# Kernel tuning notes

Measured on AMD Instinct MI355X. Metric: run time of the kernel, lower is better.

Reference implementation:

```python
import jax, jax.numpy as jnp
import numpy as np

ALPHA = 0.1
B = 500_000
EMBED = 64
HIDDEN = 128
IN_DIM = 27 + 3 + EMBED  # 94

def _gelu(x):
    return jax.nn.gelu(x, approximate=False)  # torch.nn.GELU default = exact erf

def setup_inputs() -> dict:
    key = jax.random.key(0)
    ks = jax.random.split(key, 8)
    s = 0.05
    return {
        "F": jnp.eye(3, dtype=jnp.float32)[None] + 0.1 * jax.random.normal(ks[0], (B, 3, 3), jnp.float32),
        "latent_weight": jax.random.normal(ks[1], (1024, EMBED), jnp.float32),
        "W1": s * jax.random.normal(ks[2], (IN_DIM, HIDDEN), jnp.float32), "b1": jnp.zeros((HIDDEN,), jnp.float32),
        "W2": s * jax.random.normal(ks[3], (HIDDEN, HIDDEN), jnp.float32), "b2": jnp.zeros((HIDDEN,), jnp.float32),
        "W3": s * jax.random.normal(ks[4], (HIDDEN, HIDDEN), jnp.float32), "b3": jnp.zeros((HIDDEN,), jnp.float32),
        "W4": s * jax.random.normal(ks[5], (HIDDEN, HIDDEN), jnp.float32), "b4": jnp.zeros((HIDDEN,), jnp.float32),
        "W5": s * jax.random.normal(ks[6], (HIDDEN, 9), jnp.float32), "b5": jnp.zeros((9,), jnp.float32),
        "traj_ids": jnp.asarray(7, dtype=jnp.int32),
    }

def reference(F, latent_weight, W1, b1, W2, b2, W3, b3, W4, b4, W5, b5, traj_ids):
    n = F.shape[0]
    # Batched 3x3 SVD: F = U diag(s) Vh  (torch.svd returns V; Vh = V^T here)
    U, sigma, Vh = jnp.linalg.svd(F, full_matrices=False)
    R = jnp.matmul(U, Vh)  # [n,3,3] rotation
    lat = jnp.broadcast_to(latent_weight[traj_ids][None, :], (n, latent_weight.shape[1]))
    inv = jnp.concatenate(
        [F.reshape(n, 9), U.reshape(n, 9), sigma, Vh.reshape(n, 9), lat], axis=1)  # [n, 30+embed]
    h = _gelu(inv @ W1 + b1)
    h = _gelu(h @ W2 + b2)
    h = _gelu(h @ W3 + b3)
    h = _gelu(h @ W4 + b4)
    x = (h @ W5 + b5).reshape(n, 3, 3)
    x = 0.5 * (x + jnp.swapaxes(x, 1, 2))  # symmetrize
    return ALPHA * jnp.matmul(R, x) + F
```

## Files before the change

kernel.cpp:

```cpp
#include <hip/hip_runtime.h>


typedef short bf16x8 __attribute__((ext_vector_type(8)));
typedef float f32x4 __attribute__((ext_vector_type(4)));
typedef float f32x2 __attribute__((ext_vector_type(2)));
typedef unsigned int u32x2 __attribute__((ext_vector_type(2)));
typedef unsigned short u16;

#define WS_L1     0
#define WS_L234   8192
#define WS_L5     106496
#define WS_B1EFF  110592
#define WS_B234   111104
#define WS_B5     112640
#define WS_NEEDED 131072

__device__ __forceinline__ float bf2f(u16 b){
  union { unsigned int u; float f; } v; v.u = ((unsigned int)b) << 16; return v.f;
}
__device__ __forceinline__ u16 f2bf(float f){
  union { float f; unsigned int u; } v; v.f = f;
  unsigned int x = v.u;
  return (u16)((x + 0x7fffu + ((x >> 16) & 1u)) >> 16);
}
__device__ __forceinline__ unsigned int pack2bf(float f0, float f1){
  union { float f; unsigned int u; } a, b; a.f = f0; b.f = f1;
  unsigned int u0 = a.u + 0x8000u;
  unsigned int u1 = b.u + 0x8000u;
#if __has_builtin(__builtin_amdgcn_perm)
  return __builtin_amdgcn_perm(u1, u0, 0x07060302u);
#else
  return (u0 >> 16) | (u1 & 0xffff0000u);
#endif
}
template<bool B16>
__device__ __forceinline__ float ldf(const void* p, int i){
  return B16 ? bf2f(((const u16*)p)[i]) : ((const float*)p)[i];
}
template<bool B16>
__device__ __forceinline__ short ldw(const void* p, int i){
  return B16 ? (short)((const u16*)p)[i] : (short)f2bf(((const float*)p)[i]);
}
template<bool B16>
__device__ __forceinline__ void stf(void* p, int i, float v){
  if (B16) ((u16*)p)[i] = f2bf(v); else ((float*)p)[i] = v;
}

__device__ __forceinline__ float med3f(float x, float lo, float hi){
#if __has_builtin(__builtin_amdgcn_fmed3f)
  return __builtin_amdgcn_fmed3f(x, lo, hi);
#else
  return fminf(fmaxf(x, lo), hi);
#endif
}

__device__ __forceinline__ unsigned int gelu2_pack(float x0, float x1){
  const f32x2 A7 = {-2.20713e-4f, -2.20713e-4f};
  const f32x2 A5 = { 5.86695e-3f,  5.86695e-3f};
  const f32x2 A3 = {-5.99485e-2f, -5.99485e-2f};
  const f32x2 A1 = { 3.969014e-1f, 3.969014e-1f};
  const f32x2 HF = { 0.5f, 0.5f};
  f32x2 xc; xc[0] = med3f(x0, -3.4f, 3.4f); xc[1] = med3f(x1, -3.4f, 3.4f);
  f32x2 s  = xc * xc;
  f32x2 g  = s * A7 + A5;
  g = s * g + A3;
  g = s * g + A1;
  f32x2 ph = xc * g + HF;
  f32x2 xin; xin[0] = x0; xin[1] = x1;
  f32x2 y = xin * ph;
  return pack2bf(y[0], y[1]);
}

__device__ __forceinline__ int sniff_bf16(const void* Fg){
  const u16* fu = (const u16*)Fg;
  int votes = 0;
  #pragma unroll
  for (int k = 0; k < 32; ++k){
    u16 h = fu[k*18];
    votes += (h >= 0x3E00 && h < 0x4000) ? 1 : 0;
  }
  return votes >= 16;
}

template<int P, int Q, int R3>
__device__ __forceinline__ void jrot(float bm[3][3], float v[3][3]){
  float bpq = bm[P][Q];
  if (fabsf(bpq) < 1e-30f) return;
  float th = (bm[Q][Q] - bm[P][P]) / (2.0f * bpq);
  float t = copysignf(1.0f, th) / (fabsf(th) + sqrtf(1.0f + th*th));
  float c = 1.0f / sqrtf(1.0f + t*t);
  float s = t * c;
  float bpp = bm[P][P] - t*bpq;
  float bqq = bm[Q][Q] + t*bpq;
  bm[P][P] = bpp; bm[Q][Q] = bqq; bm[P][Q] = 0.0f; bm[Q][P] = 0.0f;
  float bpr = bm[P][R3], bqr = bm[Q][R3];
  float npr = c*bpr - s*bqr;
  float nqr = s*bpr + c*bqr;
  bm[P][R3] = npr; bm[R3][P] = npr;
  bm[Q][R3] = nqr; bm[R3][Q] = nqr;
  #pragma unroll
  for (int i = 0; i < 3; ++i){
    float vp = v[i][P], vq = v[i][Q];
    v[i][P] = c*vp - s*vq;
    v[i][Q] = s*vp + c*vq;
  }
}

__device__ __forceinline__ void svd3(const float Fm[9],
                                     float u[3][3], float sg[3], float vt[3][3]){
  float bm[3][3];
  #pragma unroll
  for (int i = 0; i < 3; ++i)
    #pragma unroll
    for (int j = i; j < 3; ++j){
      float acc = Fm[0*3+i]*Fm[0*3+j] + Fm[1*3+i]*Fm[1*3+j] + Fm[2*3+i]*Fm[2*3+j];
      bm[i][j] = acc; bm[j][i] = acc;
    }
  float v[3][3] = {{1.f,0.f,0.f},{0.f,1.f,0.f},{0.f,0.f,1.f}};
  #pragma unroll
  for (int sweep = 0; sweep < 5; ++sweep){
    jrot<0,1,2>(bm, v);
    jrot<0,2,1>(bm, v);
    jrot<1,2,0>(bm, v);
  }
  float lam0 = bm[0][0], lam1 = bm[1][1], lam2 = bm[2][2];
  #define CSWAP(la, lb, A, Bc) if ((la) < (lb)) { float t_ = la; la = lb; lb = t_; \
    for (int i_ = 0; i_ < 3; ++i_){ float w_ = v[i_][A]; v[i_][A] = v[i_][Bc]; v[i_][Bc] = w_; } }
  CSWAP(lam0, lam1, 0, 1);
  CSWAP(lam0, lam2, 0, 2);
  CSWAP(lam1, lam2, 1, 2);
  #undef CSWAP
  float a[3][3];
  #pragma unroll
  for (int c = 0; c < 3; ++c)
    #pragma unroll
    for (int r = 0; r < 3; ++r)
      a[r][c] = Fm[r*3+0]*v[0][c] + Fm[r*3+1]*v[1][c] + Fm[r*3+2]*v[2][c];
  float s1 = sqrtf(a[0][0]*a[0][0] + a[1][0]*a[1][0] + a[2][0]*a[2][0]);
  float inv1 = 1.0f / fmaxf(s1, 1e-30f);
  u[0][0] = a[0][0]*inv1; u[1][0] = a[1][0]*inv1; u[2][0] = a[2][0]*inv1;
  float d12 = u[0][0]*a[0][1] + u[1][0]*a[1][1] + u[2][0]*a[2][1];
  float w20 = a[0][1] - d12*u[0][0], w21 = a[1][1] - d12*u[1][0], w22 = a[2][1] - d12*u[2][0];
  float s2 = sqrtf(w20*w20 + w21*w21 + w22*w22);
  float inv2 = 1.0f / fmaxf(s2, 1e-30f);
  u[0][1] = w20*inv2; u[1][1] = w21*inv2; u[2][1] = w22*inv2;
  float d13 = u[0][0]*a[0][2] + u[1][0]*a[1][2] + u[2][0]*a[2][2];
  float d23 = u[0][1]*a[0][2] + u[1][1]*a[1][2] + u[2][1]*a[2][2];
  float w30 = a[0][2] - d13*u[0][0] - d23*u[0][1];
  float w31 = a[1][2] - d13*u[1][0] - d23*u[1][1];
  float w32 = a[2][2] - d13*u[2][0] - d23*u[2][1];
  float s3 = sqrtf(w30*w30 + w31*w31 + w32*w32);
  if (s3 > 1e-12f){
    float inv3 = 1.0f / s3;
    u[0][2] = w30*inv3; u[1][2] = w31*inv3; u[2][2] = w32*inv3;
  } else {
    float c0 = u[1][0]*u[2][1] - u[2][0]*u[1][1];
    float c1 = u[2][0]*u[0][1] - u[0][0]*u[2][1];
    float c2 = u[0][0]*u[1][1] - u[1][0]*u[0][1];
    float dt = c0*a[0][2] + c1*a[1][2] + c2*a[2][2];
    float sgn = (dt < 0.0f) ? -1.0f : 1.0f;
    u[0][2] = c0*sgn; u[1][2] = c1*sgn; u[2][2] = c2*sgn;
    s3 = fabsf(dt);
  }
  sg[0] = s1; sg[1] = s2; sg[2] = s3;
  #pragma unroll
  for (int i = 0; i < 3; ++i)
    #pragma unroll
    for (int j = 0; j < 3; ++j)
      vt[i][j] = v[j][i];
}

template<bool B16>
__device__ void prep_body(
  const void* latg, const void* w1g, const void* b1g,
  const void* w2g, const void* b2g, const void* w3g, const void* b3g,
  const void* w4g, const void* b4g, const void* w5g, const void* b5g,
  const int* trajg, char* ws)
{
  const int tid = threadIdx.x, lane = tid & 63, wv = tid >> 6;
  const int quad = lane >> 4, l15 = lane & 15;
  const int blk = blockIdx.x;
  if (blk < 27){
    const int wr = blk*4 + wv;
    bf16x8 frag;
    if (wr < 8){
      const int ntg = wr;
      #pragma unroll
      for (int j = 0; j < 8; ++j)
        frag[j] = ldw<B16>(w1g, (quad*8 + j)*128 + ntg*16 + l15);
      *(bf16x8*)(ws + WS_L1 + (size_t)(wr*64 + lane)*16) = frag;
    } else if (wr < 104){
      const int idx = wr - 8, layer = idx >> 5, rem = idx & 31;
      const int ntg = rem >> 2, ks = rem & 3;
      const void* wg = (layer == 0) ? w2g : ((layer == 1) ? w3g : w4g);
      #pragma unroll
      for (int j = 0; j < 8; ++j)
        frag[j] = ldw<B16>(wg, (ks*32 + quad*8 + j)*128 + ntg*16 + l15);
      *(bf16x8*)(ws + WS_L234 + (size_t)(idx*64 + lane)*16) = frag;
    } else {
      const int ks = wr - 104;
      #pragma unroll
      for (int j = 0; j < 8; ++j)
        frag[j] = (l15 < 9) ? ldw<B16>(w5g, (ks*32 + quad*8 + j)*9 + l15) : (short)0;
      *(bf16x8*)(ws + WS_L5 + (size_t)(ks*64 + lane)*16) = frag;
    }
  } else {
    if (tid < 128){
      const int t7 = trajg[0];
      float acc = ldf<B16>(b1g, tid);
      for (int j = 0; j < 64; ++j)
        acc += ldf<B16>(latg, t7*64 + j) * ldf<B16>(w1g, (30 + j)*128 + tid);
      ((float*)(ws + WS_B1EFF))[tid] = acc;
    } else {
      const int n = tid - 128;
      ((float*)(ws + WS_B234))[0*128 + n] = ldf<B16>(b2g, n);
      ((float*)(ws + WS_B234))[1*128 + n] = ldf<B16>(b3g, n);
      ((float*)(ws + WS_B234))[2*128 + n] = ldf<B16>(b4g, n);
      if (n < 16) ((float*)(ws + WS_B5))[n] = (n < 9) ? ldf<B16>(b5g, n) : 0.0f;
    }
  }
}

__global__ __launch_bounds__(256)
void fproj_prep_kernel(
  const void* Fg, const void* latg, const void* w1g, const void* b1g,
  const void* w2g, const void* b2g, const void* w3g, const void* b3g,
  const void* w4g, const void* b4g, const void* w5g, const void* b5g,
  const int* __restrict__ trajg, char* ws)
{
  if (sniff_bf16(Fg))
    prep_body<true >(latg, w1g, b1g, w2g, b2g, w3g, b3g, w4g, b4g, w5g, b5g, trajg, ws);
  else
    prep_body<false>(latg, w1g, b1g, w2g, b2g, w3g, b3g, w4g, b4g, w5g, b5g, trajg, ws);
}

template<bool B16, bool WS>
__device__ __forceinline__ void mlp_layer128(
    u16 (&Hbuf)[128][136],
    const void* __restrict__ Wg, const void* __restrict__ bg,
    const char* __restrict__ wsW, const float* __restrict__ bf32,
    int wv, int lane)
{
  const int l15  = lane & 15;
  const int quad = lane >> 4;
  const int kb   = quad * 8;
  f32x4 bb[2];
  #pragma unroll
  for (int nt = 0; nt < 2; ++nt){
    const int n0 = wv*32 + nt*16 + quad*4;
    if (WS) bb[nt] = *(const f32x4*)(bf32 + n0);
    else { bb[nt][0]=ldf<B16>(bg,n0); bb[nt][1]=ldf<B16>(bg,n0+1);
           bb[nt][2]=ldf<B16>(bg,n0+2); bb[nt][3]=ldf<B16>(bg,n0+3); }
  }
  bf16x8 Wf[2][4];
  #pragma unroll
  for (int nt = 0; nt < 2; ++nt){
    const int ntg = wv*2 + nt;
    #pragma unroll
    for (int ks = 0; ks < 4; ++ks){
      if (WS){
        Wf[nt][ks] = *(const bf16x8*)(wsW + (size_t)((ntg*4 + ks)*64 + lane)*16);
      } else {
        bf16x8 bv;
        #pragma unroll
        for (int j = 0; j < 8; ++j)
          bv[j] = ldw<B16>(Wg, (ks*32 + kb + j)*128 + ntg*16 + l15);
        Wf[nt][ks] = bv;
      }
    }
  }
  f32x4 acc[8][2];
  #pragma unroll
  for (int mt = 0; mt < 8; ++mt){
    const u16* hp = &Hbuf[mt*16 + l15][kb];
    bf16x8 a0 = *(const bf16x8*)(hp);
    bf16x8 a1 = *(const bf16x8*)(hp + 32);
    bf16x8 a2 = *(const bf16x8*)(hp + 64);
    bf16x8 a3 = *(const bf16x8*)(hp + 96);
    #pragma unroll
    for (int nt = 0; nt < 2; ++nt){
      f32x4 c = bb[nt];
      c = __builtin_amdgcn_mfma_f32_16x16x32_bf16(Wf[nt][0], a0, c, 0,0,0);
      c = __builtin_amdgcn_mfma_f32_16x16x32_bf16(Wf[nt][1], a1, c, 0,0,0);
      c = __builtin_amdgcn_mfma_f32_16x16x32_bf16(Wf[nt][2], a2, c, 0,0,0);
      c = __builtin_amdgcn_mfma_f32_16x16x32_bf16(Wf[nt][3], a3, c, 0,0,0);
      acc[mt][nt] = c;
    }
  }
  __syncthreads();
  #pragma unroll
  for (int nt = 0; nt < 2; ++nt){
    const int n0 = wv*32 + nt*16 + quad*4;
    #pragma unroll
    for (int mt = 0; mt < 8; ++mt){
      f32x4 c = acc[mt][nt];
      u32x2 pk;
      pk[0] = gelu2_pack(c[0], c[1]);
      pk[1] = gelu2_pack(c[2], c[3]);
      *(u32x2*)&Hbuf[mt*16 + l15][n0] = pk;
    }
  }
  __syncthreads();
}

template<bool B16, bool WS>
__device__ void fproj_body(
  const void* Fg, const void* latg,
  const void* w1g, const void* b1g, const void* w2g, const void* b2g,
  const void* w3g, const void* b3g, const void* w4g, const void* b4g,
  const void* w5g, const void* b5g,
  const int* trajg, void* outg, int ntot, const char* ws,
  u16 (&Hbuf)[128][136], float* b1lds)
{
  const int tid  = threadIdx.x;
  const int lane = tid & 63;
  const int wv   = tid >> 6;
  const int l15  = lane & 15;
  const int quad = lane >> 4;
  const int kb   = quad * 8;
  const int row0 = blockIdx.x * 128;

  float Freg[9];
  float Rm[3][3];

  bf16x8 Wf1[2];
  #pragma unroll
  for (int nt = 0; nt < 2; ++nt){
    const int ntg = wv*2 + nt;
    if (WS){
      Wf1[nt] = *(const bf16x8*)(ws + WS_L1 + (size_t)(ntg*64 + lane)*16);
    } else {
      bf16x8 bv;
      #pragma unroll
      for (int j = 0; j < 8; ++j)
        bv[j] = ldw<B16>(w1g, (kb + j)*128 + ntg*16 + l15);
      Wf1[nt] = bv;
    }
  }

  if (tid < 128){
    const int r = row0 + tid;
    float fv[32];
    if (r < ntot){
      float A0[9];
      #pragma unroll
      for (int k = 0; k < 9; ++k){ A0[k] = ldf<B16>(Fg, r*9 + k); Freg[k] = A0[k]; }
      float uu[3][3], ss[3], vvt[3][3];
      svd3(A0, uu, ss, vvt);
      #pragma unroll
      for (int i = 0; i < 3; ++i)
        #pragma unroll
        for (int j = 0; j < 3; ++j)
          Rm[i][j] = uu[i][0]*vvt[0][j] + uu[i][1]*vvt[1][j] + uu[i][2]*vvt[2][j];
      #pragma unroll
      for (int k = 0; k < 9; ++k) fv[k]    = A0[k];
      #pragma unroll
      for (int k = 0; k < 9; ++k) fv[9+k]  = uu[k/3][k%3];
      fv[18] = ss[0]; fv[19] = ss[1]; fv[20] = ss[2];
      #pragma unroll
      for (int k = 0; k < 9; ++k) fv[21+k] = vvt[k/3][k%3];
      fv[30] = 0.0f; fv[31] = 0.0f;
    } else {
      #pragma unroll
      for (int k = 0; k < 32; ++k) fv[k] = 0.0f;
      #pragma unroll
      for (int k = 0; k < 9; ++k) Freg[k] = 0.0f;
      #pragma unroll
      for (int i = 0; i < 3; ++i)
        #pragma unroll
        for (int j = 0; j < 3; ++j) Rm[i][j] = 0.0f;
    }
    #pragma unroll
    for (int q = 0; q < 4; ++q){
      u32x2 pk;
      pk[0] = pack2bf(fv[q*8+0], fv[q*8+1]);
      pk[1] = pack2bf(fv[q*8+2], fv[q*8+3]);
      *(u32x2*)&Hbuf[tid][q*8 + 0] = pk;
      pk[0] = pack2bf(fv[q*8+4], fv[q*8+5]);
      pk[1] = pack2bf(fv[q*8+6], fv[q*8+7]);
      *(u32x2*)&Hbuf[tid][q*8 + 4] = pk;
    }
  } else if (!WS){
    const int n = tid - 128;
    const int t7 = trajg[0];
    float acc = ldf<B16>(b1g, n);
    for (int j = 0; j < 64; ++j)
      acc += ldf<B16>(latg, t7*64 + j) * ldf<B16>(w1g, (30 + j)*128 + n);
    b1lds[n] = acc;
  }
  __syncthreads();

  {
    f32x4 bb[2];
    #pragma unroll
    for (int nt = 0; nt < 2; ++nt){
      const int n0 = wv*32 + nt*16 + quad*4;
      if (WS) bb[nt] = *(const f32x4*)((const float*)(ws + WS_B1EFF) + n0);
      else { bb[nt][0]=b1lds[n0]; bb[nt][1]=b1lds[n0+1]; bb[nt][2]=b1lds[n0+2]; bb[nt][3]=b1lds[n0+3]; }
    }
    f32x4 acc[8][2];
    #pragma unroll
    for (int mt = 0; mt < 8; ++mt){
      bf16x8 av = *(const bf16x8*)&Hbuf[mt*16 + l15][kb];
      #pragma unroll
      for (int nt = 0; nt < 2; ++nt){
        f32x4 c = bb[nt];
        c = __builtin_amdgcn_mfma_f32_16x16x32_bf16(Wf1[nt], av, c, 0,0,0);
        acc[mt][nt] = c;
      }
    }
    __syncthreads();
    #pragma unroll
    for (int nt = 0; nt < 2; ++nt){
      const int n0 = wv*32 + nt*16 + quad*4;
      #pragma unroll
      for (int mt = 0; mt < 8; ++mt){
        f32x4 c = acc[mt][nt];
        u32x2 pk;
        pk[0] = gelu2_pack(c[0], c[1]);
        pk[1] = gelu2_pack(c[2], c[3]);
        *(u32x2*)&Hbuf[mt*16 + l15][n0] = pk;
      }
    }
  }
  __syncthreads();

  const float* bf32 = (const float*)(ws + WS_B234);
  mlp_layer128<B16,WS>(Hbuf, w2g, b2g, ws + WS_L234 + 0*32768, bf32 + 0*128, wv, lane);
  mlp_layer128<B16,WS>(Hbuf, w3g, b3g, ws + WS_L234 + 1*32768, bf32 + 1*128, wv, lane);
  mlp_layer128<B16,WS>(Hbuf, w4g, b4g, ws + WS_L234 + 2*32768, bf32 + 2*128, wv, lane);

  {
    bf16x8 W5f[4];
    #pragma unroll
    for (int ks = 0; ks < 4; ++ks){
      if (WS){
        W5f[ks] = *(const bf16x8*)(ws + WS_L5 + (size_t)(ks*64 + lane)*16);
      } else {
        bf16x8 bv;
        #pragma unroll
        for (int j = 0; j < 8; ++j)
          bv[j] = (l15 < 9) ? ldw<B16>(w5g, (ks*32 + kb + j)*9 + l15) : (short)0;
        W5f[ks] = bv;
      }
    }
    f32x4 bb5;
    if (WS) bb5 = *(const f32x4*)((const float*)(ws + WS_B5) + quad*4);
    else {
      #pragma unroll
      for (int rg = 0; rg < 4; ++rg)
        bb5[rg] = (quad*4 + rg < 9) ? ldf<B16>(b5g, quad*4 + rg) : 0.0f;
    }
    #pragma unroll
    for (int t = 0; t < 2; ++t){
      const int mt = wv*2 + t;
      const u16* hp = &Hbuf[mt*16 + l15][kb];
      bf16x8 a0 = *(const bf16x8*)(hp);
      bf16x8 a1 = *(const bf16x8*)(hp + 32);
      bf16x8 a2 = *(const bf16x8*)(hp + 64);
      bf16x8 a3 = *(const bf16x8*)(hp + 96);
      f32x4 c = bb5;
      c = __builtin_amdgcn_mfma_f32_16x16x32_bf16(W5f[0], a0, c, 0,0,0);
      c = __builtin_amdgcn_mfma_f32_16x16x32_bf16(W5f[1], a1, c, 0,0,0);
      c = __builtin_amdgcn_mfma_f32_16x16x32_bf16(W5f[2], a2, c, 0,0,0);
      c = __builtin_amdgcn_mfma_f32_16x16x32_bf16(W5f[3], a3, c, 0,0,0);
      *(f32x4*)((float*)&Hbuf[mt*16 + l15][0] + quad*4) = c;
    }
  }
  __syncthreads();

  if (tid < 128){
    const int r = row0 + tid;
    if (r < ntot){
      const float* xr = (const float*)&Hbuf[tid][0];
      float x[9];
      #pragma unroll
      for (int k = 0; k < 9; ++k) x[k] = xr[k];
      float xs[3][3];
      #pragma unroll
      for (int i = 0; i < 3; ++i)
        #pragma unroll
        for (int j = 0; j < 3; ++j)
          xs[i][j] = 0.5f*(x[i*3+j] + x[j*3+i]);
      #pragma unroll
      for (int i = 0; i < 3; ++i)
        #pragma unroll
        for (int j = 0; j < 3; ++j){
          float y = Rm[i][0]*xs[0][j] + Rm[i][1]*xs[1][j] + Rm[i][2]*xs[2][j];
          stf<B16>(outg, r*9 + i*3 + j, 0.1f*y + Freg[i*3+j]);
        }
    }
  }
}

__global__ __launch_bounds__(256, 4)
void fproj_ws_kernel(
  const void* Fg, const void* latg,
  const void* w1g, const void* b1g, const void* w2g, const void* b2g,
  const void* w3g, const void* b3g, const void* w4g, const void* b4g,
  const void* w5g, const void* b5g,
  const int* __restrict__ trajg, void* outg, int ntot, const char* ws)
{
  __shared__ alignas(16) u16 Hbuf[128][136];
  if (sniff_bf16(Fg))
    fproj_body<true , true>(Fg, latg, w1g, b1g, w2g, b2g, w3g, b3g, w4g, b4g,
                            w5g, b5g, trajg, outg, ntot, ws, Hbuf, nullptr);
  else
    fproj_body<false, true>(Fg, latg, w1g, b1g, w2g, b2g, w3g, b3g, w4g, b4g,
                            w5g, b5g, trajg, outg, ntot, ws, Hbuf, nullptr);
}

__global__ __launch_bounds__(256, 4)
void fproj_plain_kernel(
  const void* Fg, const void* latg,
  const void* w1g, const void* b1g, const void* w2g, const void* b2g,
  const void* w3g, const void* b3g, const void* w4g, const void* b4g,
  const void* w5g, const void* b5g,
  const int* __restrict__ trajg, void* outg, int ntot)
{
  __shared__ alignas(16) u16 Hbuf[128][136];
  __shared__ float b1lds[128];
  if (sniff_bf16(Fg))
    fproj_body<true , false>(Fg, latg, w1g, b1g, w2g, b2g, w3g, b3g, w4g, b4g,
                             w5g, b5g, trajg, outg, ntot, nullptr, Hbuf, b1lds);
  else
    fproj_body<false, false>(Fg, latg, w1g, b1g, w2g, b2g, w3g, b3g, w4g, b4g,
                             w5g, b5g, trajg, outg, ntot, nullptr, Hbuf, b1lds);
}

extern "C" void kernel_launch(void* const* d_in, const int* in_sizes, int n_in,
                              void* d_out, int out_size, void* d_ws, size_t ws_size,
                              hipStream_t stream) {
  (void)n_in; (void)out_size;
  const int n = in_sizes[0] / 9;
  dim3 grid((n + 127) / 128), block(256);
  if (ws_size >= (size_t)WS_NEEDED){
    hipLaunchKernelGGL(fproj_prep_kernel, dim3(28), block, 0, stream,
      (const void*)d_in[0],  (const void*)d_in[1],
      (const void*)d_in[2],  (const void*)d_in[3],
      (const void*)d_in[4],  (const void*)d_in[5],
      (const void*)d_in[6],  (const void*)d_in[7],
      (const void*)d_in[8],  (const void*)d_in[9],
      (const void*)d_in[10], (const void*)d_in[11],
      (const int*)d_in[12], (char*)d_ws);
    hipLaunchKernelGGL(fproj_ws_kernel, grid, block, 0, stream,
      (const void*)d_in[0],  (const void*)d_in[1],
      (const void*)d_in[2],  (const void*)d_in[3],
      (const void*)d_in[4],  (const void*)d_in[5],
      (const void*)d_in[6],  (const void*)d_in[7],
      (const void*)d_in[8],  (const void*)d_in[9],
      (const void*)d_in[10], (const void*)d_in[11],
      (const int*)d_in[12], d_out, n, (const char*)d_ws);
  } else {
    hipLaunchKernelGGL(fproj_plain_kernel, grid, block, 0, stream,
      (const void*)d_in[0],  (const void*)d_in[1],
      (const void*)d_in[2],  (const void*)d_in[3],
      (const void*)d_in[4],  (const void*)d_in[5],
      (const void*)d_in[6],  (const void*)d_in[7],
      (const void*)d_in[8],  (const void*)d_in[9],
      (const void*)d_in[10], (const void*)d_in[11],
      (const int*)d_in[12], d_out, n);
  }
}
```

Baseline: 198.6 us.

## Replace padded LDS activation buffer with XOR-swizzled unpadded layout

The activation tile in LDS drops its 8-element row padding (136 to 128 columns). Bank conflicts are now avoided by XOR-swizzling 16-byte chunks with the row index, applied to every read and write of the buffer. The smaller LDS footprint lets the launch-bounds occupancy hint rise from 4 to 5 blocks per CU, and the GELU clamp now uses vector min/max builtins instead of fmed3. The risk is extra address arithmetic and higher register pressure under the tighter occupancy bound.

```diff
diff --git a/kernel.cpp b/kernel.cpp
--- a/kernel.cpp
+++ b/kernel.cpp
@@ -46,12 +46,8 @@
   if (B16) ((u16*)p)[i] = f2bf(v); else ((float*)p)[i] = v;
 }
 
-__device__ __forceinline__ float med3f(float x, float lo, float hi){
-#if __has_builtin(__builtin_amdgcn_fmed3f)
-  return __builtin_amdgcn_fmed3f(x, lo, hi);
-#else
-  return fminf(fmaxf(x, lo), hi);
-#endif
+__device__ __forceinline__ int swz(int r15, int boff){
+  return boff ^ (r15 << 4);
 }
 
 __device__ __forceinline__ unsigned int gelu2_pack(float x0, float x1){
@@ -60,13 +56,15 @@
   const f32x2 A3 = {-5.99485e-2f, -5.99485e-2f};
   const f32x2 A1 = { 3.969014e-1f, 3.969014e-1f};
   const f32x2 HF = { 0.5f, 0.5f};
-  f32x2 xc; xc[0] = med3f(x0, -3.4f, 3.4f); xc[1] = med3f(x1, -3.4f, 3.4f);
+  const f32x2 LO = {-3.4f, -3.4f};
+  const f32x2 HI = { 3.4f,  3.4f};
+  f32x2 xin; xin[0] = x0; xin[1] = x1;
+  f32x2 xc = __builtin_elementwise_max(LO, __builtin_elementwise_min(xin, HI));
   f32x2 s  = xc * xc;
   f32x2 g  = s * A7 + A5;
   g = s * g + A3;
   g = s * g + A1;
   f32x2 ph = xc * g + HF;
-  f32x2 xin; xin[0] = x0; xin[1] = x1;
   f32x2 y = xin * ph;
   return pack2bf(y[0], y[1]);
 }
@@ -236,7 +234,7 @@
 
 template<bool B16, bool WS>
 __device__ __forceinline__ void mlp_layer128(
-    u16 (&Hbuf)[128][136],
+    u16 (&Hbuf)[128][128],
     const void* __restrict__ Wg, const void* __restrict__ bg,
     const char* __restrict__ wsW, const float* __restrict__ bf32,
     int wv, int lane)
@@ -272,11 +270,11 @@
   f32x4 acc[8][2];
   #pragma unroll
   for (int mt = 0; mt < 8; ++mt){
-    const u16* hp = &Hbuf[mt*16 + l15][kb];
-    bf16x8 a0 = *(const bf16x8*)(hp);
-    bf16x8 a1 = *(const bf16x8*)(hp + 32);
-    bf16x8 a2 = *(const bf16x8*)(hp + 64);
-    bf16x8 a3 = *(const bf16x8*)(hp + 96);
+    const char* rb = (const char*)&Hbuf[mt*16 + l15][0];
+    bf16x8 a0 = *(const bf16x8*)(rb + swz(l15, quad*16 +   0));
+    bf16x8 a1 = *(const bf16x8*)(rb + swz(l15, quad*16 +  64));
+    bf16x8 a2 = *(const bf16x8*)(rb + swz(l15, quad*16 + 128));
+    bf16x8 a3 = *(const bf16x8*)(rb + swz(l15, quad*16 + 192));
     #pragma unroll
     for (int nt = 0; nt < 2; ++nt){
       f32x4 c = bb[nt];
@@ -290,14 +288,14 @@
   __syncthreads();
   #pragma unroll
   for (int nt = 0; nt < 2; ++nt){
-    const int n0 = wv*32 + nt*16 + quad*4;
+    const int boff = wv*64 + nt*32 + quad*8;
     #pragma unroll
     for (int mt = 0; mt < 8; ++mt){
       f32x4 c = acc[mt][nt];
       u32x2 pk;
       pk[0] = gelu2_pack(c[0], c[1]);
       pk[1] = gelu2_pack(c[2], c[3]);
-      *(u32x2*)&Hbuf[mt*16 + l15][n0] = pk;
+      *(u32x2*)((char*)&Hbuf[mt*16 + l15][0] + swz(l15, boff)) = pk;
     }
   }
   __syncthreads();
@@ -310,7 +308,7 @@
   const void* w3g, const void* b3g, const void* w4g, const void* b4g,
   const void* w5g, const void* b5g,
   const int* trajg, void* outg, int ntot, const char* ws,
-  u16 (&Hbuf)[128][136], float* b1lds)
+  u16 (&Hbuf)[128][128], float* b1lds)
 {
   const int tid  = threadIdx.x;
   const int lane = tid & 63;
@@ -370,15 +368,17 @@
         #pragma unroll
         for (int j = 0; j < 3; ++j) Rm[i][j] = 0.0f;
     }
+    char* rb = (char*)&Hbuf[tid][0];
+    const int r15 = tid & 15;
     #pragma unroll
     for (int q = 0; q < 4; ++q){
       u32x2 pk;
       pk[0] = pack2bf(fv[q*8+0], fv[q*8+1]);
       pk[1] = pack2bf(fv[q*8+2], fv[q*8+3]);
-      *(u32x2*)&Hbuf[tid][q*8 + 0] = pk;
+      *(u32x2*)(rb + swz(r15, q*16 + 0)) = pk;
       pk[0] = pack2bf(fv[q*8+4], fv[q*8+5]);
       pk[1] = pack2bf(fv[q*8+6], fv[q*8+7]);
-      *(u32x2*)&Hbuf[tid][q*8 + 4] = pk;
+      *(u32x2*)(rb + swz(r15, q*16 + 8)) = pk;
     }
   } else if (!WS){
     const int n = tid - 128;
@@ -401,7 +401,8 @@
     f32x4 acc[8][2];
     #pragma unroll
     for (int mt = 0; mt < 8; ++mt){
-      bf16x8 av = *(const bf16x8*)&Hbuf[mt*16 + l15][kb];
+      const char* rb = (const char*)&Hbuf[mt*16 + l15][0];
+      bf16x8 av = *(const bf16x8*)(rb + swz(l15, quad*16));
       #pragma unroll
       for (int nt = 0; nt < 2; ++nt){
         f32x4 c = bb[nt];
@@ -412,14 +413,14 @@
     __syncthreads();
     #pragma unroll
     for (int nt = 0; nt < 2; ++nt){
-      const int n0 = wv*32 + nt*16 + quad*4;
+      const int boff = wv*64 + nt*32 + quad*8;
       #pragma unroll
       for (int mt = 0; mt < 8; ++mt){
         f32x4 c = acc[mt][nt];
         u32x2 pk;
         pk[0] = gelu2_pack(c[0], c[1]);
         pk[1] = gelu2_pack(c[2], c[3]);
-        *(u32x2*)&Hbuf[mt*16 + l15][n0] = pk;
+        *(u32x2*)((char*)&Hbuf[mt*16 + l15][0] + swz(l15, boff)) = pk;
       }
     }
   }
@@ -454,17 +455,17 @@
     #pragma unroll
     for (int t = 0; t < 2; ++t){
       const int mt = wv*2 + t;
-      const u16* hp = &Hbuf[mt*16 + l15][kb];
-      bf16x8 a0 = *(const bf16x8*)(hp);
-      bf16x8 a1 = *(const bf16x8*)(hp + 32);
-      bf16x8 a2 = *(const bf16x8*)(hp + 64);
-      bf16x8 a3 = *(const bf16x8*)(hp + 96);
+      char* rb = (char*)&Hbuf[mt*16 + l15][0];
+      bf16x8 a0 = *(const bf16x8*)(rb + swz(l15, quad*16 +   0));
+      bf16x8 a1 = *(const bf16x8*)(rb + swz(l15, quad*16 +  64));
+      bf16x8 a2 = *(const bf16x8*)(rb + swz(l15, quad*16 + 128));
+      bf16x8 a3 = *(const bf16x8*)(rb + swz(l15, quad*16 + 192));
       f32x4 c = bb5;
       c = __builtin_amdgcn_mfma_f32_16x16x32_bf16(W5f[0], a0, c, 0,0,0);
       c = __builtin_amdgcn_mfma_f32_16x16x32_bf16(W5f[1], a1, c, 0,0,0);
       c = __builtin_amdgcn_mfma_f32_16x16x32_bf16(W5f[2], a2, c, 0,0,0);
       c = __builtin_amdgcn_mfma_f32_16x16x32_bf16(W5f[3], a3, c, 0,0,0);
-      *(f32x4*)((float*)&Hbuf[mt*16 + l15][0] + quad*4) = c;
+      *(f32x4*)(rb + swz(l15, quad*16)) = c;
     }
   }
   __syncthreads();
@@ -472,10 +473,14 @@
   if (tid < 128){
     const int r = row0 + tid;
     if (r < ntot){
-      const float* xr = (const float*)&Hbuf[tid][0];
+      const char* rb = (const char*)&Hbuf[tid][0];
+      const int r15 = tid & 15;
       float x[9];
-      #pragma unroll
-      for (int k = 0; k < 9; ++k) x[k] = xr[k];
+      f32x4 x03 = *(const f32x4*)(rb + swz(r15, 0));
+      f32x4 x47 = *(const f32x4*)(rb + swz(r15, 16));
+      x[0]=x03[0]; x[1]=x03[1]; x[2]=x03[2]; x[3]=x03[3];
+      x[4]=x47[0]; x[5]=x47[1]; x[6]=x47[2]; x[7]=x47[3];
+      x[8] = *(const float*)(rb + swz(r15, 32));
       float xs[3][3];
       #pragma unroll
       for (int i = 0; i < 3; ++i)
@@ -493,7 +498,7 @@
   }
 }
 
-__global__ __launch_bounds__(256, 4)
+__global__ __launch_bounds__(256, 5)
 void fproj_ws_kernel(
   const void* Fg, const void* latg,
   const void* w1g, const void* b1g, const void* w2g, const void* b2g,
@@ -501,7 +506,7 @@
   const void* w5g, const void* b5g,
   const int* __restrict__ trajg, void* outg, int ntot, const char* ws)
 {
-  __shared__ alignas(16) u16 Hbuf[128][136];
+  __shared__ alignas(16) u16 Hbuf[128][128];
   if (sniff_bf16(Fg))
     fproj_body<true , true>(Fg, latg, w1g, b1g, w2g, b2g, w3g, b3g, w4g, b4g,
                             w5g, b5g, trajg, outg, ntot, ws, Hbuf, nullptr);
@@ -518,7 +523,7 @@
   const void* w5g, const void* b5g,
   const int* __restrict__ trajg, void* outg, int ntot)
 {
-  __shared__ alignas(16) u16 Hbuf[128][136];
+  __shared__ alignas(16) u16 Hbuf[128][128];
   __shared__ float b1lds[128];
   if (sniff_bf16(Fg))
     fproj_body<true , false>(Fg, latg, w1g, b1g, w2g, b2g, w3g, b3g, w4g, b4g,
```

New measurement: 248.7 us. 25.2% more time.
